# Performance work log

Measured on AMD Instinct MI355X. Metric: run time of the kernel, lower is better.

The kernel has to match this reference:

```python
import jax, jax.numpy as jnp
import numpy as np

N = 100_000   # nodes
E = 1_600_000 # edges
F = 32        # input features
G = 512       # graphs in batch
EPS = 1e-5    # batchnorm eps


def setup_inputs() -> dict:
    key = jax.random.key(0)
    ks = jax.random.split(key, 24)
    d = {
        "x": jax.random.normal(ks[0], (N, F), jnp.float32),
        "edge_index": jax.random.randint(ks[1], (2, E), 0, N),
        "batch": jnp.sort(jax.random.randint(ks[2], (N,), 0, G)),
        "Wl1": jax.random.normal(ks[3], (30, F), jnp.float32) * 0.1,
        "bl1": jax.random.normal(ks[4], (30,), jnp.float32) * 0.1,
        "Wr1": jax.random.normal(ks[5], (30, F), jnp.float32) * 0.1,
        "Wl2": jax.random.normal(ks[6], (30, 30), jnp.float32) * 0.1,
        "bl2": jax.random.normal(ks[7], (30,), jnp.float32) * 0.1,
        "Wr2": jax.random.normal(ks[8], (30, 30), jnp.float32) * 0.1,
        "g1": jax.random.uniform(ks[9], (30,), jnp.float32) + 0.5,
        "b1": jax.random.normal(ks[10], (30,), jnp.float32) * 0.1,
        "m1": jax.random.normal(ks[11], (30,), jnp.float32) * 0.1,
        "v1": jax.random.uniform(ks[12], (30,), jnp.float32) + 0.5,
        "g2": jax.random.uniform(ks[13], (30,), jnp.float32) + 0.5,
        "b2": jax.random.normal(ks[14], (30,), jnp.float32) * 0.1,
        "m2": jax.random.normal(ks[15], (30,), jnp.float32) * 0.1,
        "v2": jax.random.uniform(ks[16], (30,), jnp.float32) + 0.5,
        "W1": jax.random.normal(ks[17], (10, 60), jnp.float32) * 0.1,
        "bb1": jax.random.normal(ks[18], (10,), jnp.float32) * 0.1,
        "W2": jax.random.normal(ks[19], (1, 10), jnp.float32) * 0.1,
        "bb2": jax.random.normal(ks[20], (1,), jnp.float32) * 0.1,
    }
    return d


def reference(x, edge_index, batch, Wl1, bl1, Wr1, Wl2, bl2, Wr2,
              g1, b1, m1, v1, g2, b2, m2, v2, W1, bb1, W2, bb2):
    src, dst = edge_index[0], edge_index[1]

    def sage(h, Wl, bl, Wr):
        # mean aggregation of source features into targets (PyG SAGEConv default)
        s = jax.ops.segment_sum(h[src], dst, num_segments=N)
        cnt = jax.ops.segment_sum(jnp.ones((E,), h.dtype), dst, num_segments=N)
        agg = s / jnp.maximum(cnt, 1.0)[:, None]
        return agg @ Wl.T + bl + h @ Wr.T

    def bn(h, g, b, m, v):  # BatchNorm1d, eval mode (running stats)
        return (h - m) * jax.lax.rsqrt(v + EPS) * g + b

    h = bn(jax.nn.relu(sage(x, Wl1, bl1, Wr1)), g1, b1, m1, v1)
    h = bn(jax.nn.relu(sage(h, Wl2, bl2, Wr2)), g2, b2, m2, v2)

    # dual segment pooling over graphs
    xmax = jax.ops.segment_max(h, batch, num_segments=G)
    xmax = jnp.where(jnp.isfinite(xmax), xmax, 0.0)  # empty graphs -> 0
    s = jax.ops.segment_sum(h, batch, num_segments=G)
    c = jax.ops.segment_sum(jnp.ones((N,), h.dtype), batch, num_segments=G)
    xmean = s / jnp.maximum(c, 1.0)[:, None]

    z = jnp.concatenate([xmax, xmean], axis=1)  # [G, 60]
    z = jax.nn.relu(z @ W1.T + bb1)
    z = z @ W2.T + bb2
    return jax.nn.sigmoid(z)  # [G, 1]
```

## Files before the change

### kernel.cpp

```cpp
#include <hip/hip_runtime.h>
#include <hip/hip_fp16.h>

#define NN 100000
#define NE 1600000
#define FI 32
#define FH 30
#define PAD 32
#define NG 512
#define NBK 782
#define BNODES 128
#define SCB 1024
#define CBLK 32
#define NCHUNK (SCB / CBLK)
#define CAP 4096
#define NB1 391
#define F8B 3125

__global__ __launch_bounds__(256) void k_phist(const int* __restrict__ dst,
                                               unsigned short* __restrict__ partial,
                                               const float* __restrict__ x, unsigned* __restrict__ x8)
{
    __shared__ int cnt[NBK];
    if (blockIdx.x >= SCB) {
        int i = (blockIdx.x - SCB) * 256 + threadIdx.x;
        if (i < NN * 8) {
            float4 f = ((const float4*)x)[i];
            unsigned w = 0;
            w = __builtin_amdgcn_cvt_pk_fp8_f32(f.x, f.y, w, false);
            w = __builtin_amdgcn_cvt_pk_fp8_f32(f.z, f.w, w, true);
            x8[i] = w;
        }
        return;
    }
    for (int i = threadIdx.x; i < NBK; i += 256) cnt[i] = 0;
    __syncthreads();
    for (int e = blockIdx.x * 256 + threadIdx.x; e < NE; e += SCB * 256)
        atomicAdd(&cnt[dst[e] >> 7], 1);
    __syncthreads();
    for (int i = threadIdx.x; i < NBK; i += 256)
        partial[(size_t)blockIdx.x * NBK + i] = (unsigned short)cnt[i];
}

__global__ __launch_bounds__(256) void k_csum(const unsigned short* __restrict__ partial,
                                              int* __restrict__ chunksum)
{
    int t = blockIdx.x * 256 + threadIdx.x;
    if (t >= NCHUNK * NBK) return;
    int c = t / NBK, b = t - c * NBK;
    int s = 0;
    #pragma unroll 8
    for (int k = 0; k < CBLK; ++k)
        s += partial[(size_t)(c * CBLK + k) * NBK + b];
    chunksum[c * NBK + b] = s;
}

__global__ __launch_bounds__(1024) void k_cscan(const int* __restrict__ chunksum,
                                                int* __restrict__ chunkbase, int* __restrict__ bktOff)
{
    __shared__ int tmp[1024];
    int tid = threadIdx.x;
    int cs[NCHUNK];
    int total = 0;
    if (tid < NBK) {
        #pragma unroll
        for (int c = 0; c < NCHUNK; ++c) { cs[c] = chunksum[c * NBK + tid]; total += cs[c]; }
    }
    tmp[tid] = (tid < NBK) ? total : 0;
    __syncthreads();
    for (int off = 1; off < 1024; off <<= 1) {
        int t = (tid >= off) ? tmp[tid - off] : 0;
        __syncthreads();
        tmp[tid] += t;
        __syncthreads();
    }
    if (tid < NBK) {
        bktOff[tid] = tmp[tid] - total;
        int run = 0;
        #pragma unroll
        for (int c = 0; c < NCHUNK; ++c) { chunkbase[c * NBK + tid] = run; run += cs[c]; }
    }
    if (tid == 0) bktOff[NBK] = NE;
}

__global__ __launch_bounds__(256) void k_base(unsigned short* __restrict__ partial,
                                              const int* __restrict__ chunkbase)
{
    int t = blockIdx.x * 256 + threadIdx.x;
    if (t >= NCHUNK * NBK) return;
    int c = t / NBK, b = t - c * NBK;
    int run = chunkbase[c * NBK + b];
    #pragma unroll 8
    for (int k = 0; k < CBLK; ++k) {
        size_t idx = (size_t)(c * CBLK + k) * NBK + b;
        int v = partial[idx];
        partial[idx] = (unsigned short)run;
        run += v;
    }
}

__global__ __launch_bounds__(256) void k_bscat(const int* __restrict__ src, const int* __restrict__ dst,
                                               const unsigned short* __restrict__ partial,
                                               const int* __restrict__ bktOff,
                                               unsigned* __restrict__ pairs)
{
    __shared__ int sbase[NBK];
    __shared__ int scnt[NBK];
    for (int i = threadIdx.x; i < NBK; i += 256) {
        sbase[i] = bktOff[i] + (int)partial[(size_t)blockIdx.x * NBK + i];
        scnt[i] = 0;
    }
    __syncthreads();
    for (int e = blockIdx.x * 256 + threadIdx.x; e < NE; e += SCB * 256) {
        int d = dst[e];
        int b = d >> 7;
        int r = atomicAdd(&scnt[b], 1);
        pairs[sbase[b] + r] = ((unsigned)src[e] << 7) | (unsigned)(d & 127);
    }
}

__global__ __launch_bounds__(256) void k_csr(
    const int* __restrict__ bktOff, const unsigned* __restrict__ pairs,
    int* __restrict__ rowstart, int* __restrict__ col)
{
    __shared__ unsigned sp[CAP];
    __shared__ int bins[BNODES], binpos[BNODES], stmp[BNODES];
    int tid = threadIdx.x;
    int bkt = blockIdx.x;
    int gbase = bktOff[bkt];
    int cnt = bktOff[bkt + 1] - gbase;
    if (tid < BNODES) bins[tid] = 0;
    __syncthreads();
    bool inl = (cnt <= CAP);
    if (inl) {
        for (int i = tid; i < cnt; i += 256) {
            unsigned u = pairs[gbase + i];
            sp[i] = u;
            atomicAdd(&bins[u & 127], 1);
        }
    } else {
        for (int i = tid; i < cnt; i += 256)
            atomicAdd(&bins[pairs[gbase + i] & 127], 1);
    }
    __syncthreads();
    if (tid < BNODES) stmp[tid] = bins[tid];
    __syncthreads();
    for (int off = 1; off < BNODES; off <<= 1) {
        int t = 0;
        if (tid < BNODES && tid >= off) t = stmp[tid - off];
        __syncthreads();
        if (tid < BNODES) stmp[tid] += t;
        __syncthreads();
    }
    if (tid < BNODES) {
        int ex = stmp[tid] - bins[tid];
        binpos[tid] = ex;
        int n = (bkt << 7) + tid;
        if (n < NN) rowstart[n] = gbase + ex;
        if (bkt == 0 && tid == 0) rowstart[NN] = NE;
    }
    __syncthreads();
    if (inl) {
        for (int i = tid; i < cnt; i += 256) {
            unsigned u = sp[i];
            int p = atomicAdd(&binpos[u & 127], 1);
            col[gbase + p] = (int)(u >> 7);
        }
    } else {
        for (int i = tid; i < cnt; i += 256) {
            unsigned u = pairs[gbase + i];
            int p = atomicAdd(&binpos[u & 127], 1);
            col[gbase + p] = (int)(u >> 7);
        }
    }
}

__global__ __launch_bounds__(256) void k_agg8(const int* __restrict__ rowstart,
                                              const int* __restrict__ col,
                                              const uint2* __restrict__ hin,
                                              float* __restrict__ aggout)
{
    int tid = blockIdx.x * 256 + threadIdx.x;
    int n = tid >> 6;
    if (n >= NN) return;
    int lane = threadIdx.x & 63;
    int q = lane & 3;
    int grp = lane >> 2;
    int rs = rowstart[n], re = rowstart[n + 1];
    float a0 = 0.0f, a1 = 0.0f, a2 = 0.0f, a3 = 0.0f;
    float a4 = 0.0f, a5 = 0.0f, a6 = 0.0f, a7 = 0.0f;
    for (int e = rs + grp; e < re; e += 16) {
        uint2 u = hin[(size_t)col[e] * 4 + q];
        auto f0 = __builtin_amdgcn_cvt_pk_f32_fp8(u.x, false);
        auto f1 = __builtin_amdgcn_cvt_pk_f32_fp8(u.x, true);
        auto f2 = __builtin_amdgcn_cvt_pk_f32_fp8(u.y, false);
        auto f3 = __builtin_amdgcn_cvt_pk_f32_fp8(u.y, true);
        a0 += f0[0]; a1 += f0[1]; a2 += f1[0]; a3 += f1[1];
        a4 += f2[0]; a5 += f2[1]; a6 += f3[0]; a7 += f3[1];
    }
    #pragma unroll
    for (int off = 4; off < 64; off <<= 1) {
        a0 += __shfl_xor(a0, off); a1 += __shfl_xor(a1, off);
        a2 += __shfl_xor(a2, off); a3 += __shfl_xor(a3, off);
        a4 += __shfl_xor(a4, off); a5 += __shfl_xor(a5, off);
        a6 += __shfl_xor(a6, off); a7 += __shfl_xor(a7, off);
    }
    if (lane < 4) {
        float inv = (re > rs) ? 1.0f / (float)(re - rs) : 0.0f;
        float4* o = (float4*)(aggout + (size_t)n * PAD + q * 8);
        o[0] = make_float4(a0 * inv, a1 * inv, a2 * inv, a3 * inv);
        o[1] = make_float4(a4 * inv, a5 * inv, a6 * inv, a7 * inv);
    }
}

__global__ __launch_bounds__(256) void k_t1(
    const float* __restrict__ x, const float* __restrict__ agg,
    const float* __restrict__ Wl, const float* __restrict__ bl, const float* __restrict__ Wr,
    const float* __restrict__ g, const float* __restrict__ b,
    const float* __restrict__ m, const float* __restrict__ v,
    unsigned* __restrict__ h1_8)
{
    __shared__ float sWl[FH * FI], sWr[FH * FI], sBias[FH], sScale[FH], sShift[FH];
    for (int i = threadIdx.x; i < FH * FI; i += 256) { sWl[i] = Wl[i]; sWr[i] = Wr[i]; }
    if (threadIdx.x < FH) {
        int j = threadIdx.x;
        float sc = g[j] * rsqrtf(v[j] + 1e-5f);
        sBias[j] = bl[j];
        sScale[j] = sc;
        sShift[j] = b[j] - m[j] * sc;
    }
    __syncthreads();
    int n = blockIdx.x * 256 + threadIdx.x;
    if (n >= NN) return;
    float xr[FI], ar[FI];
    #pragma unroll
    for (int k = 0; k < FI; k += 4) {
        float4 xv = *(const float4*)(x + (size_t)n * FI + k);
        float4 av = *(const float4*)(agg + (size_t)n * PAD + k);
        xr[k] = xv.x; xr[k+1] = xv.y; xr[k+2] = xv.z; xr[k+3] = xv.w;
        ar[k] = av.x; ar[k+1] = av.y; ar[k+2] = av.z; ar[k+3] = av.w;
    }
    float res[32];
    for (int j = 0; j < FH; ++j) {
        float acc = sBias[j];
        #pragma unroll
        for (int k = 0; k < FI; ++k)
            acc += ar[k] * sWl[j * FI + k] + xr[k] * sWr[j * FI + k];
        acc = fmaxf(acc, 0.0f);
        res[j] = acc * sScale[j] + sShift[j];
    }
    res[30] = 0.0f; res[31] = 0.0f;
    unsigned* row = h1_8 + (size_t)n * 8;
    #pragma unroll
    for (int w = 0; w < 8; ++w) {
        unsigned pw = 0;
        pw = __builtin_amdgcn_cvt_pk_fp8_f32(res[4*w],   res[4*w+1], pw, false);
        pw = __builtin_amdgcn_cvt_pk_fp8_f32(res[4*w+2], res[4*w+3], pw, true);
        row[w] = pw;
    }
}

__global__ __launch_bounds__(256) void k_t2(
    const unsigned* __restrict__ h1_8, const float* __restrict__ agg,
    const float* __restrict__ Wl, const float* __restrict__ bl, const float* __restrict__ Wr,
    const float* __restrict__ g, const float* __restrict__ b,
    const float* __restrict__ m, const float* __restrict__ v,
    __half2* __restrict__ h2h)
{
    __shared__ float sWl[FH * FH], sWr[FH * FH], sBias[FH], sScale[FH], sShift[FH];
    for (int i = threadIdx.x; i < FH * FH; i += 256) { sWl[i] = Wl[i]; sWr[i] = Wr[i]; }
    if (threadIdx.x < FH) {
        int j = threadIdx.x;
        float sc = g[j] * rsqrtf(v[j] + 1e-5f);
        sBias[j] = bl[j];
        sScale[j] = sc;
        sShift[j] = b[j] - m[j] * sc;
    }
    __syncthreads();
    int n = blockIdx.x * 256 + threadIdx.x;
    if (n >= NN) return;
    float xr[32], ar[FH];
    const unsigned* hrow = h1_8 + (size_t)n * 8;
    #pragma unroll
    for (int w = 0; w < 8; ++w) {
        unsigned u = hrow[w];
        auto lo = __builtin_amdgcn_cvt_pk_f32_fp8(u, false);
        auto hi = __builtin_amdgcn_cvt_pk_f32_fp8(u, true);
        xr[4*w] = lo[0]; xr[4*w+1] = lo[1]; xr[4*w+2] = hi[0]; xr[4*w+3] = hi[1];
    }
    #pragma unroll
    for (int k = 0; k < FH; ++k)
        ar[k] = agg[(size_t)n * PAD + k];
    float res[FH];
    for (int j = 0; j < FH; ++j) {
        float acc = sBias[j];
        #pragma unroll
        for (int k = 0; k < FH; ++k)
            acc += ar[k] * sWl[j * FH + k] + xr[k] * sWr[j * FH + k];
        acc = fmaxf(acc, 0.0f);
        res[j] = acc * sScale[j] + sShift[j];
    }
    __half2* row = h2h + (size_t)n * (PAD / 2);
    #pragma unroll
    for (int j = 0; j < FH; j += 2)
        row[j >> 1] = __floats2half2_rn(res[j], res[j + 1]);
}

__global__ __launch_bounds__(256) void k_pool(
    const __half* __restrict__ h2, const int* __restrict__ batch,
    const float* __restrict__ W1, const float* __restrict__ bb1,
    const float* __restrict__ W2, const float* __restrict__ bb2,
    float* __restrict__ out)
{
    __shared__ float sS[8][FH], sM[8][FH], sz[2 * FH], st[10];
    int tid = threadIdx.x;
    int gi = blockIdx.x;
    int lo = 0, hi = NN;
    while (lo < hi) { int mid = (lo + hi) >> 1; if (batch[mid] < gi) lo = mid + 1; else hi = mid; }
    int start = lo;
    hi = NN;
    while (lo < hi) { int mid = (lo + hi) >> 1; if (batch[mid] <= gi) lo = mid + 1; else hi = mid; }
    int end = lo;

    int f = tid & 31;
    int ng = tid >> 5;
    float sum = 0.0f, mx = -INFINITY;
    if (f < FH) {
        for (int n = start + ng; n < end; n += 8) {
            float val = __half2float(h2[(size_t)n * PAD + f]);
            sum += val;
            mx = fmaxf(mx, val);
        }
        sS[ng][f] = sum;
        sM[ng][f] = mx;
    }
    __syncthreads();
    if (tid < FH) {
        float s = 0.0f, mm = -INFINITY;
        #pragma unroll
        for (int w = 0; w < 8; ++w) { s += sS[w][tid]; mm = fmaxf(mm, sM[w][tid]); }
        int c = end - start;
        sz[tid]      = (c > 0) ? mm : 0.0f;
        sz[FH + tid] = (c > 0) ? s / (float)c : 0.0f;
    }
    __syncthreads();
    if (tid < 10) {
        float t = bb1[tid];
        for (int k = 0; k < 2 * FH; ++k) t += sz[k] * W1[tid * 2 * FH + k];
        st[tid] = fmaxf(t, 0.0f);
    }
    __syncthreads();
    if (tid == 0) {
        float o = bb2[0];
        for (int j = 0; j < 10; ++j) o += st[j] * W2[j];
        out[gi] = 1.0f / (1.0f + expf(-o));
    }
}

extern "C" void kernel_launch(void* const* d_in, const int* in_sizes, int n_in,
                              void* d_out, int out_size, void* d_ws, size_t ws_size,
                              hipStream_t stream)
{
    const float* x   = (const float*)d_in[0];
    const int*   ei  = (const int*)d_in[1];
    const int*   bat = (const int*)d_in[2];
    const float* Wl1 = (const float*)d_in[3];
    const float* bl1 = (const float*)d_in[4];
    const float* Wr1 = (const float*)d_in[5];
    const float* Wl2 = (const float*)d_in[6];
    const float* bl2 = (const float*)d_in[7];
    const float* Wr2 = (const float*)d_in[8];
    const float* g1  = (const float*)d_in[9];
    const float* b1  = (const float*)d_in[10];
    const float* m1  = (const float*)d_in[11];
    const float* v1  = (const float*)d_in[12];
    const float* g2  = (const float*)d_in[13];
    const float* b2  = (const float*)d_in[14];
    const float* m2  = (const float*)d_in[15];
    const float* v2  = (const float*)d_in[16];
    const float* W1  = (const float*)d_in[17];
    const float* bb1 = (const float*)d_in[18];
    const float* W2  = (const float*)d_in[19];
    const float* bb2 = (const float*)d_in[20];

    const int* src = ei;
    const int* dst = ei + NE;

    unsigned short* partial = (unsigned short*)d_ws;
    int* chunksum  = (int*)((char*)d_ws + (size_t)SCB * NBK * 2);
    int* chunkbase = chunksum + NCHUNK * NBK;
    int* bktOff    = chunkbase + NCHUNK * NBK;
    int* rowstart  = bktOff + NBK + 2;
    unsigned* pairs = (unsigned*)(rowstart + NN + 4);
    int* col       = (int*)(pairs + NE);
    unsigned* x8   = (unsigned*)(col + NE);
    unsigned* h1_8 = x8 + (size_t)NN * 8;
    __half2*  h2h  = (__half2*)(h1_8 + (size_t)NN * 8);
    float* aggbuf  = (float*)(h2h + (size_t)NN * (PAD / 2));

    int pb = (NCHUNK * NBK + 255) / 256;

    k_phist <<<SCB + F8B, 256, 0, stream>>>(dst, partial, x, x8);
    k_csum  <<<pb, 256, 0, stream>>>(partial, chunksum);
    k_cscan <<<1, 1024, 0, stream>>>(chunksum, chunkbase, bktOff);
    k_base  <<<pb, 256, 0, stream>>>(partial, chunkbase);
    k_bscat <<<SCB, 256, 0, stream>>>(src, dst, partial, bktOff, pairs);
    k_csr   <<<NBK, 256, 0, stream>>>(bktOff, pairs, rowstart, col);

    int ab = (NN * 64 + 255) / 256;
    k_agg8<<<ab, 256, 0, stream>>>(rowstart, col, (const uint2*)x8, aggbuf);
    k_t1<<<NB1, 256, 0, stream>>>(x, aggbuf, Wl1, bl1, Wr1, g1, b1, m1, v1, h1_8);
    k_agg8<<<ab, 256, 0, stream>>>(rowstart, col, (const uint2*)h1_8, aggbuf);
    k_t2<<<NB1, 256, 0, stream>>>(h1_8, aggbuf, Wl2, bl2, Wr2, g2, b2, m2, v2, h2h);
    k_pool<<<NG, 256, 0, stream>>>((const __half*)h2h, bat, W1, bb1, W2, bb2, (float*)d_out);
}
```

Baseline: 190.9 us.

## Fuse prefix-scan stages cooperatively, store aggregates in fp16, fold layer-2 transform into pooling

Three prefix-sum kernels are replaced by one cooperative kernel that uses a grid-wide sync. The aggregation output is stored as fp16 instead of fp32, halving that buffer's traffic. The second SAGE transform kernel is removed and its work is done inside the per-graph pooling kernel, so the h2 tensor is never written or read back. The cost is lower precision, per-iteration block syncs inside pooling with only 512 blocks, and bktOff[NBK] is now computed as a total rather than set to NE.

Result: slower. 230.8 us (+20.9%).

```diff
diff --git a/kernel.cpp b/kernel.cpp
--- a/kernel.cpp
+++ b/kernel.cpp
@@ -1,5 +1,6 @@
 #include <hip/hip_runtime.h>
 #include <hip/hip_fp16.h>
+#include <hip/hip_cooperative_groups.h>
 
 #define NN 100000
 #define NE 1600000
@@ -15,6 +16,7 @@
 #define CAP 4096
 #define NB1 391
 #define F8B 3125
+#define PFB 98
 
 __global__ __launch_bounds__(256) void k_phist(const int* __restrict__ dst,
                                                unsigned short* __restrict__ partial,
@@ -41,60 +43,52 @@
         partial[(size_t)blockIdx.x * NBK + i] = (unsigned short)cnt[i];
 }
 
-__global__ __launch_bounds__(256) void k_csum(const unsigned short* __restrict__ partial,
-                                              int* __restrict__ chunksum)
-{
+__global__ __launch_bounds__(256) void k_prefix(unsigned short* __restrict__ partial,
+                                                int* __restrict__ chunksum,
+                                                int* __restrict__ bktOff)
+{
+    cooperative_groups::grid_group grid = cooperative_groups::this_grid();
     int t = blockIdx.x * 256 + threadIdx.x;
-    if (t >= NCHUNK * NBK) return;
-    int c = t / NBK, b = t - c * NBK;
-    int s = 0;
-    #pragma unroll 8
-    for (int k = 0; k < CBLK; ++k)
-        s += partial[(size_t)(c * CBLK + k) * NBK + b];
-    chunksum[c * NBK + b] = s;
-}
-
-__global__ __launch_bounds__(1024) void k_cscan(const int* __restrict__ chunksum,
-                                                int* __restrict__ chunkbase, int* __restrict__ bktOff)
-{
-    __shared__ int tmp[1024];
-    int tid = threadIdx.x;
-    int cs[NCHUNK];
-    int total = 0;
-    if (tid < NBK) {
-        #pragma unroll
-        for (int c = 0; c < NCHUNK; ++c) { cs[c] = chunksum[c * NBK + tid]; total += cs[c]; }
-    }
-    tmp[tid] = (tid < NBK) ? total : 0;
-    __syncthreads();
-    for (int off = 1; off < 1024; off <<= 1) {
-        int t = (tid >= off) ? tmp[tid - off] : 0;
+    int c = t / NBK, b = t - (t / NBK) * NBK;
+    if (t < NCHUNK * NBK) {
+        int s = 0;
+        #pragma unroll 8
+        for (int k = 0; k < CBLK; ++k)
+            s += partial[(size_t)(c * CBLK + k) * NBK + b];
+        chunksum[c * NBK + b] = s;
+    }
+    grid.sync();
+    if (blockIdx.x == 0) {
+        __shared__ int tot[NBK];
+        int tid = threadIdx.x;
+        for (int i = tid; i < NBK; i += 256) {
+            int s = 0;
+            for (int cc = 0; cc < NCHUNK; ++cc) s += chunksum[cc * NBK + i];
+            tot[i] = s;
+        }
         __syncthreads();
-        tmp[tid] += t;
-        __syncthreads();
-    }
-    if (tid < NBK) {
-        bktOff[tid] = tmp[tid] - total;
+        for (int off = 1; off < NBK; off <<= 1) {
+            int vals[(NBK + 255) / 256];
+            for (int i = tid, j = 0; i < NBK; i += 256, ++j)
+                vals[j] = (i >= off) ? tot[i - off] : 0;
+            __syncthreads();
+            for (int i = tid, j = 0; i < NBK; i += 256, ++j)
+                tot[i] += vals[j];
+            __syncthreads();
+        }
+        for (int i = tid; i < NBK; i += 256) bktOff[i + 1] = tot[i];
+        if (tid == 0) bktOff[0] = 0;
+    }
+    if (t < NCHUNK * NBK) {
         int run = 0;
-        #pragma unroll
-        for (int c = 0; c < NCHUNK; ++c) { chunkbase[c * NBK + tid] = run; run += cs[c]; }
-    }
-    if (tid == 0) bktOff[NBK] = NE;
-}
-
-__global__ __launch_bounds__(256) void k_base(unsigned short* __restrict__ partial,
-                                              const int* __restrict__ chunkbase)
-{
-    int t = blockIdx.x * 256 + threadIdx.x;
-    if (t >= NCHUNK * NBK) return;
-    int c = t / NBK, b = t - c * NBK;
-    int run = chunkbase[c * NBK + b];
-    #pragma unroll 8
-    for (int k = 0; k < CBLK; ++k) {
-        size_t idx = (size_t)(c * CBLK + k) * NBK + b;
-        int v = partial[idx];
-        partial[idx] = (unsigned short)run;
-        run += v;
+        for (int cc = 0; cc < c; ++cc) run += chunksum[cc * NBK + b];
+        #pragma unroll 8
+        for (int k = 0; k < CBLK; ++k) {
+            size_t idx = (size_t)(c * CBLK + k) * NBK + b;
+            int vv = partial[idx];
+            partial[idx] = (unsigned short)run;
+            run += vv;
+        }
     }
 }
 
@@ -177,7 +171,7 @@
 __global__ __launch_bounds__(256) void k_agg8(const int* __restrict__ rowstart,
                                               const int* __restrict__ col,
                                               const uint2* __restrict__ hin,
-                                              float* __restrict__ aggout)
+                                              __half2* __restrict__ aggh)
 {
     int tid = blockIdx.x * 256 + threadIdx.x;
     int n = tid >> 6;
@@ -206,14 +200,17 @@
     }
     if (lane < 4) {
         float inv = (re > rs) ? 1.0f / (float)(re - rs) : 0.0f;
-        float4* o = (float4*)(aggout + (size_t)n * PAD + q * 8);
-        o[0] = make_float4(a0 * inv, a1 * inv, a2 * inv, a3 * inv);
-        o[1] = make_float4(a4 * inv, a5 * inv, a6 * inv, a7 * inv);
+        union { __half2 h[4]; uint4 u; } pk;
+        pk.h[0] = __floats2half2_rn(a0 * inv, a1 * inv);
+        pk.h[1] = __floats2half2_rn(a2 * inv, a3 * inv);
+        pk.h[2] = __floats2half2_rn(a4 * inv, a5 * inv);
+        pk.h[3] = __floats2half2_rn(a6 * inv, a7 * inv);
+        ((uint4*)(aggh + (size_t)n * 16))[q] = pk.u;
     }
 }
 
 __global__ __launch_bounds__(256) void k_t1(
-    const float* __restrict__ x, const float* __restrict__ agg,
+    const float* __restrict__ x, const __half2* __restrict__ aggh,
     const float* __restrict__ Wl, const float* __restrict__ bl, const float* __restrict__ Wr,
     const float* __restrict__ g, const float* __restrict__ b,
     const float* __restrict__ m, const float* __restrict__ v,
@@ -235,9 +232,13 @@
     #pragma unroll
     for (int k = 0; k < FI; k += 4) {
         float4 xv = *(const float4*)(x + (size_t)n * FI + k);
-        float4 av = *(const float4*)(agg + (size_t)n * PAD + k);
         xr[k] = xv.x; xr[k+1] = xv.y; xr[k+2] = xv.z; xr[k+3] = xv.w;
-        ar[k] = av.x; ar[k+1] = av.y; ar[k+2] = av.z; ar[k+3] = av.w;
+    }
+    const __half2* arow = aggh + (size_t)n * 16;
+    #pragma unroll
+    for (int k2 = 0; k2 < 16; ++k2) {
+        float2 fv = __half22float2(arow[k2]);
+        ar[2 * k2] = fv.x; ar[2 * k2 + 1] = fv.y;
     }
     float res[32];
     for (int j = 0; j < FH; ++j) {
@@ -259,60 +260,32 @@
     }
 }
 
-__global__ __launch_bounds__(256) void k_t2(
-    const unsigned* __restrict__ h1_8, const float* __restrict__ agg,
+__global__ __launch_bounds__(256) void k_pool(
+    const unsigned* __restrict__ h1_8, const __half2* __restrict__ aggh,
+    const int* __restrict__ batch,
     const float* __restrict__ Wl, const float* __restrict__ bl, const float* __restrict__ Wr,
     const float* __restrict__ g, const float* __restrict__ b,
     const float* __restrict__ m, const float* __restrict__ v,
-    __half2* __restrict__ h2h)
-{
-    __shared__ float sWl[FH * FH], sWr[FH * FH], sBias[FH], sScale[FH], sShift[FH];
-    for (int i = threadIdx.x; i < FH * FH; i += 256) { sWl[i] = Wl[i]; sWr[i] = Wr[i]; }
-    if (threadIdx.x < FH) {
-        int j = threadIdx.x;
-        float sc = g[j] * rsqrtf(v[j] + 1e-5f);
-        sBias[j] = bl[j];
-        sScale[j] = sc;
-        sShift[j] = b[j] - m[j] * sc;
-    }
-    __syncthreads();
-    int n = blockIdx.x * 256 + threadIdx.x;
-    if (n >= NN) return;
-    float xr[32], ar[FH];
-    const unsigned* hrow = h1_8 + (size_t)n * 8;
-    #pragma unroll
-    for (int w = 0; w < 8; ++w) {
-        unsigned u = hrow[w];
-        auto lo = __builtin_amdgcn_cvt_pk_f32_fp8(u, false);
-        auto hi = __builtin_amdgcn_cvt_pk_f32_fp8(u, true);
-        xr[4*w] = lo[0]; xr[4*w+1] = lo[1]; xr[4*w+2] = hi[0]; xr[4*w+3] = hi[1];
-    }
-    #pragma unroll
-    for (int k = 0; k < FH; ++k)
-        ar[k] = agg[(size_t)n * PAD + k];
-    float res[FH];
-    for (int j = 0; j < FH; ++j) {
-        float acc = sBias[j];
-        #pragma unroll
-        for (int k = 0; k < FH; ++k)
-            acc += ar[k] * sWl[j * FH + k] + xr[k] * sWr[j * FH + k];
-        acc = fmaxf(acc, 0.0f);
-        res[j] = acc * sScale[j] + sShift[j];
-    }
-    __half2* row = h2h + (size_t)n * (PAD / 2);
-    #pragma unroll
-    for (int j = 0; j < FH; j += 2)
-        row[j >> 1] = __floats2half2_rn(res[j], res[j + 1]);
-}
-
-__global__ __launch_bounds__(256) void k_pool(
-    const __half* __restrict__ h2, const int* __restrict__ batch,
     const float* __restrict__ W1, const float* __restrict__ bb1,
     const float* __restrict__ W2, const float* __restrict__ bb2,
     float* __restrict__ out)
 {
+    __shared__ float sWl[FH * 33], sWr[FH * 33], sBias[FH], sScale[FH], sShift[FH];
+    __shared__ float sAgg[8][33], sSelf[8][33];
     __shared__ float sS[8][FH], sM[8][FH], sz[2 * FH], st[10];
     int tid = threadIdx.x;
+    for (int i = tid; i < FH * FH; i += 256) {
+        int j = i / FH, k = i - j * FH;
+        sWl[j * 33 + k] = Wl[i];
+        sWr[j * 33 + k] = Wr[i];
+    }
+    if (tid < FH) {
+        float sc = g[tid] * rsqrtf(v[tid] + 1e-5f);
+        sBias[tid] = bl[tid];
+        sScale[tid] = sc;
+        sShift[tid] = b[tid] - m[tid] * sc;
+    }
+    __syncthreads();
     int gi = blockIdx.x;
     int lo = 0, hi = NN;
     while (lo < hi) { int mid = (lo + hi) >> 1; if (batch[mid] < gi) lo = mid + 1; else hi = mid; }
@@ -324,23 +297,48 @@
     int f = tid & 31;
     int ng = tid >> 5;
     float sum = 0.0f, mx = -INFINITY;
-    if (f < FH) {
-        for (int n = start + ng; n < end; n += 8) {
-            float val = __half2float(h2[(size_t)n * PAD + f]);
+    int cnt = end - start;
+    int iters = (cnt + 7) >> 3;
+    for (int it = 0; it < iters; ++it) {
+        int n = start + (it << 3) + ng;
+        bool valid = (n < end);
+        if (valid) {
+            if (f < 16) {
+                float2 fv = __half22float2(aggh[(size_t)n * 16 + f]);
+                sAgg[ng][2 * f]     = fv.x;
+                sAgg[ng][2 * f + 1] = fv.y;
+            } else if (f < 24) {
+                int w = f - 16;
+                unsigned u = h1_8[(size_t)n * 8 + w];
+                auto lo2 = __builtin_amdgcn_cvt_pk_f32_fp8(u, false);
+                auto hi2 = __builtin_amdgcn_cvt_pk_f32_fp8(u, true);
+                sSelf[ng][4 * w]     = lo2[0];
+                sSelf[ng][4 * w + 1] = lo2[1];
+                sSelf[ng][4 * w + 2] = hi2[0];
+                sSelf[ng][4 * w + 3] = hi2[1];
+            }
+        }
+        __syncthreads();
+        if (valid && f < FH) {
+            float acc = sBias[f];
+            #pragma unroll
+            for (int k = 0; k < FH; ++k)
+                acc += sAgg[ng][k] * sWl[f * 33 + k] + sSelf[ng][k] * sWr[f * 33 + k];
+            acc = fmaxf(acc, 0.0f);
+            float val = acc * sScale[f] + sShift[f];
             sum += val;
             mx = fmaxf(mx, val);
         }
-        sS[ng][f] = sum;
-        sM[ng][f] = mx;
-    }
+        __syncthreads();
+    }
+    if (f < FH) { sS[ng][f] = sum; sM[ng][f] = mx; }
     __syncthreads();
     if (tid < FH) {
         float s = 0.0f, mm = -INFINITY;
         #pragma unroll
         for (int w = 0; w < 8; ++w) { s += sS[w][tid]; mm = fmaxf(mm, sM[w][tid]); }
-        int c = end - start;
-        sz[tid]      = (c > 0) ? mm : 0.0f;
-        sz[FH + tid] = (c > 0) ? s / (float)c : 0.0f;
+        sz[tid]      = (cnt > 0) ? mm : 0.0f;
+        sz[FH + tid] = (cnt > 0) ? s / (float)cnt : 0.0f;
     }
     __syncthreads();
     if (tid < 10) {
@@ -387,29 +385,31 @@
 
     unsigned short* partial = (unsigned short*)d_ws;
     int* chunksum  = (int*)((char*)d_ws + (size_t)SCB * NBK * 2);
-    int* chunkbase = chunksum + NCHUNK * NBK;
-    int* bktOff    = chunkbase + NCHUNK * NBK;
+    int* bktOff    = chunksum + NCHUNK * NBK;
     int* rowstart  = bktOff + NBK + 2;
     unsigned* pairs = (unsigned*)(rowstart + NN + 4);
     int* col       = (int*)(pairs + NE);
     unsigned* x8   = (unsigned*)(col + NE);
     unsigned* h1_8 = x8 + (size_t)NN * 8;
-    __half2*  h2h  = (__half2*)(h1_8 + (size_t)NN * 8);
-    float* aggbuf  = (float*)(h2h + (size_t)NN * (PAD / 2));
-
-    int pb = (NCHUNK * NBK + 255) / 256;
-
-    k_phist <<<SCB + F8B, 256, 0, stream>>>(dst, partial, x, x8);
-    k_csum  <<<pb, 256, 0, stream>>>(partial, chunksum);
-    k_cscan <<<1, 1024, 0, stream>>>(chunksum, chunkbase, bktOff);
-    k_base  <<<pb, 256, 0, stream>>>(partial, chunkbase);
-    k_bscat <<<SCB, 256, 0, stream>>>(src, dst, partial, bktOff, pairs);
-    k_csr   <<<NBK, 256, 0, stream>>>(bktOff, pairs, rowstart, col);
+    __half2*  aggh = (__half2*)(h1_8 + (size_t)NN * 8);
+
+    k_phist<<<SCB + F8B, 256, 0, stream>>>(dst, partial, x, x8);
+
+    {
+        unsigned short* a0 = partial;
+        int* a1 = chunksum;
+        int* a2 = bktOff;
+        void* args[] = { (void*)&a0, (void*)&a1, (void*)&a2 };
+        hipLaunchCooperativeKernel((void*)k_prefix, dim3(PFB), dim3(256), args, 0, stream);
+    }
+
+    k_bscat<<<SCB, 256, 0, stream>>>(src, dst, partial, bktOff, pairs);
+    k_csr  <<<NBK, 256, 0, stream>>>(bktOff, pairs, rowstart, col);
 
     int ab = (NN * 64 + 255) / 256;
-    k_agg8<<<ab, 256, 0, stream>>>(rowstart, col, (const uint2*)x8, aggbuf);
-    k_t1<<<NB1, 256, 0, stream>>>(x, aggbuf, Wl1, bl1, Wr1, g1, b1, m1, v1, h1_8);
-    k_agg8<<<ab, 256, 0, stream>>>(rowstart, col, (const uint2*)h1_8, aggbuf);
-    k_t2<<<NB1, 256, 0, stream>>>(h1_8, aggbuf, Wl2, bl2, Wr2, g2, b2, m2, v2, h2h);
-    k_pool<<<NG, 256, 0, stream>>>((const __half*)h2h, bat, W1, bb1, W2, bb2, (float*)d_out);
-}
+    k_agg8<<<ab, 256, 0, stream>>>(rowstart, col, (const uint2*)x8, aggh);
+    k_t1<<<NB1, 256, 0, stream>>>(x, aggh, Wl1, bl1, Wr1, g1, b1, m1, v1, h1_8);
+    k_agg8<<<ab, 256, 0, stream>>>(rowstart, col, (const uint2*)h1_8, aggh);
+    k_pool<<<NG, 256, 0, stream>>>(h1_8, aggh, bat, Wl2, bl2, Wr2, g2, b2, m2, v2,
+                                   W1, bb1, W2, bb2, (float*)d_out);
+}
```
